# Performance work log

Hardware: AMD Instinct MI355X
Metric: run time of the kernel (lower is better)

Reference implementation:

```python
import jax, jax.numpy as jnp
import numpy as np

B, S, D = 64, 1024, 1024
NUM_TAGS = 33            # real IOBES tags
N = NUM_TAGS + 1         # + BOS tag
BOS = N - 1
NEG_INF = -10000.0


def setup_inputs() -> dict:
    key = jax.random.key(0)
    k1, k2, k3, k4 = jax.random.split(key, 4)
    emissions = jax.random.normal(k1, (B, S, D), dtype=jnp.float32)
    tags = jax.random.randint(k2, (B, S), 0, NUM_TAGS)          # valid real tags only
    mask = jnp.ones((B, S), dtype=jnp.float32)
    W = jax.random.normal(k3, (D, N), dtype=jnp.float32) / np.sqrt(D)
    b = jnp.zeros((N,), dtype=jnp.float32)
    transitions = jax.random.uniform(k4, (N, N), minval=-0.1, maxval=0.1, dtype=jnp.float32)
    # nothing may transition INTO the BOS tag
    transitions = transitions.at[:, BOS].set(NEG_INF)
    return {"emissions": emissions, "tags": tags, "mask": mask,
            "W": W, "b": b, "transitions": transitions}


def _crf_nll(em, tags, mask, transitions):
    """em: (B,S,N) projected emissions. Returns scalar NLL (sum over batch)."""
    # ---- gold path score ----
    first = tags[:, 0]                                          # (B,)
    score = transitions[BOS, first] + jnp.take_along_axis(em[:, 0], first[:, None], axis=1)[:, 0]
    e_t = jnp.take_along_axis(em[:, 1:], tags[:, 1:, None], axis=2)[..., 0]   # (B,S-1)
    t_t = transitions[tags[:, :-1], tags[:, 1:]]                 # (B,S-1)
    score = score + jnp.sum((e_t + t_t) * mask[:, 1:], axis=1)   # (B,)

    # ---- log partition via forward algorithm (scan over time) ----
    alphas0 = transitions[BOS][None, :] + em[:, 0]               # (B,N)

    def step(alphas, xs):
        em_t, m_t = xs                                           # (B,N), (B,)
        # scores[b, prev, nxt] = alphas[b,prev] + T[prev,nxt] + em_t[b,nxt]
        scores = alphas[:, :, None] + transitions[None] + em_t[:, None, :]
        new = jax.scipy.special.logsumexp(scores, axis=1)        # (B,N)
        m = m_t[:, None]
        return m * new + (1.0 - m) * alphas, None

    xs = (jnp.swapaxes(em[:, 1:], 0, 1), jnp.swapaxes(mask[:, 1:], 0, 1))  # time-major
    alphas, _ = jax.lax.scan(step, alphas0, xs)
    partition = jax.scipy.special.logsumexp(alphas, axis=1)      # (B,)
    return -jnp.sum(score - partition)


def reference(emissions, tags, mask, W, b, transitions):
    proj = emissions @ W + b                                     # (B,S,N), dropout p=0 is identity
    loss = _crf_nll(proj, tags, mask, transitions)
    logits = proj[:, :, :-1]                                     # drop BOS column, as in torch forward
    return loss, logits
```

## Files before the change

kernel.cpp:

```cpp
#include <hip/hip_runtime.h>
#include <math.h>

#define SS 1024
#define DD 1024
#define NB 64
#define NT 34
#define NP 48
#define NC 32
#define BOSR 33

typedef __attribute__((ext_vector_type(8))) short bf16x8;
typedef __attribute__((ext_vector_type(4))) float f32x4;

#define WS_BOS   0
#define WS_PMAT  (WS_BOS + NB*SS)
#define WS_CC    (WS_PMAT + NB*NC*NP*NP)
#define WS_Z     (WS_CC + NB*NC)
#define WS_SC    (WS_Z + NB)
#define WS_CNT   (WS_SC + NB)
#define WS_BF16  (WS_CNT + 1)
#define BW_WT    0
#define BW_ETA   (48*1024)

__device__ __forceinline__ float warp_sum64(float x) {
  #pragma unroll
  for (int off = 32; off > 0; off >>= 1) x += __shfl_down(x, off, 64);
  return x;
}
__device__ __forceinline__ float rfl(float x) {
  return __int_as_float(__builtin_amdgcn_readfirstlane(__float_as_int(x)));
}
__device__ __forceinline__ unsigned short f2bf(float f) {
  unsigned int u = __float_as_uint(f);
  unsigned int r = u + 0x7fffu + ((u >> 16) & 1u);
  return (unsigned short)(r >> 16);
}
__device__ __forceinline__ float bf2f(unsigned short h) {
  return __uint_as_float(((unsigned int)h) << 16);
}
__device__ __forceinline__ unsigned int pk_bf16(float a, float b) {
  unsigned int d;
  asm("v_cvt_pk_bf16_f32 %0, %1, %2" : "=v"(d) : "v"(a), "v"(b));
  return d;
}
__device__ __forceinline__ void lds_barrier() {
  asm volatile("s_waitcnt lgkmcnt(0)" ::: "memory");
  __builtin_amdgcn_s_barrier();
  __builtin_amdgcn_sched_barrier(0);
}

__global__ __launch_bounds__(256) void prep(const float* __restrict__ W,
                                            const float* __restrict__ T,
                                            unsigned short* __restrict__ bw,
                                            int* __restrict__ cnt) {
  int idx = blockIdx.x * 256 + threadIdx.x;
  if (idx == 0) *cnt = 0;
  if (idx < 48 * 1024) {
    int n = idx >> 10, k = idx & 1023;
    float v = (n < NT) ? W[k * NT + n] : 0.0f;
    bw[BW_WT + idx] = f2bf(v);
  } else if (idx < 48 * 1024 + 48 * 64) {
    int j = idx - 48 * 1024;
    int m = j >> 6, k = j & 63;
    float v = (m < NT && k < NT) ? __expf(T[k * NT + m]) : 0.0f;
    bw[BW_ETA + j] = f2bf(v);
  }
}

__global__ __launch_bounds__(256) void gemm_chains(
    const float* __restrict__ em, const unsigned short* __restrict__ bw,
    const float* __restrict__ bias, const float* __restrict__ mask,
    float* __restrict__ logits, float* __restrict__ bos,
    float* __restrict__ Pmat, float* __restrict__ CC) {
  union SMem {
    unsigned short At[2][128][40];
    struct {
      unsigned short S[4][48][72];
      float eeL[4][32][52];
    } ch;
  };
  __shared__ __align__(16) SMem sm;
  const int tid = threadIdx.x;
  const int lane = tid & 63, wv = tid >> 6;
  const int q = lane >> 4, l15 = lane & 15;
  const size_t row0 = (size_t)blockIdx.x * 128;
  const int b = (int)(row0 >> 10);
  const int cg = (((int)(row0 & 1023)) >> 5) + wv;
  const unsigned short* Wt = bw + BW_WT;
  const f32x4* g4 = (const f32x4*)(em + row0 * DD);

  f32x4 acc[2][3];
  f32x4 z4 = {0.f, 0.f, 0.f, 0.f};
  #pragma unroll
  for (int mt = 0; mt < 2; ++mt)
    #pragma unroll
    for (int nt = 0; nt < 3; ++nt) acc[mt][nt] = z4;

  int sr[4], sq[4];
  #pragma unroll
  for (int i = 0; i < 4; ++i) { int s = tid + i * 256; sr[i] = s >> 3; sq[i] = s & 7; }

  f32x4 pf[4];
  #pragma unroll
  for (int i = 0; i < 4; ++i)
    pf[i] = __builtin_nontemporal_load(g4 + sr[i] * 256 + sq[i]);
  bf16x8 Bf[3], Bn[3];
  #pragma unroll
  for (int nt = 0; nt < 3; ++nt)
    Bf[nt] = *(const bf16x8*)(Wt + (nt * 16 + l15) * 1024 + q * 8);

  for (int c = 0; c < 32; ++c) {
    #pragma unroll
    for (int i = 0; i < 4; ++i) {
      uint2 pk;
      pk.x = pk_bf16(pf[i][0], pf[i][1]);
      pk.y = pk_bf16(pf[i][2], pf[i][3]);
      *(uint2*)&sm.At[c & 1][sr[i]][sq[i] * 4] = pk;
    }
    int cn = (c + 1 < 32) ? c + 1 : c;
    #pragma unroll
    for (int i = 0; i < 4; ++i)
      pf[i] = __builtin_nontemporal_load(g4 + sr[i] * 256 + cn * 8 + sq[i]);
    #pragma unroll
    for (int nt = 0; nt < 3; ++nt)
      Bn[nt] = *(const bf16x8*)(Wt + (nt * 16 + l15) * 1024 + cn * 32 + q * 8);
    lds_barrier();
    bf16x8 Af[2];
    #pragma unroll
    for (int mt = 0; mt < 2; ++mt)
      Af[mt] = *(const bf16x8*)&sm.At[c & 1][wv * 32 + mt * 16 + l15][q * 8];
    #pragma unroll
    for (int mt = 0; mt < 2; ++mt)
      #pragma unroll
      for (int nt = 0; nt < 3; ++nt)
        acc[mt][nt] = __builtin_amdgcn_mfma_f32_16x16x32_bf16(
            Af[mt], Bf[nt], acc[mt][nt], 0, 0, 0);
    #pragma unroll
    for (int nt = 0; nt < 3; ++nt) Bf[nt] = Bn[nt];
  }

  __syncthreads();

  #pragma unroll
  for (int nt = 0; nt < 3; ++nt) {
    int col = nt * 16 + l15;
    float bj = (col < NT) ? bias[col] : 0.0f;
    #pragma unroll
    for (int mt = 0; mt < 2; ++mt) {
      #pragma unroll
      for (int r = 0; r < 4; ++r) {
        float v = acc[mt][nt][r] + bj;
        size_t rg = row0 + wv * 32 + mt * 16 + q * 4 + r;
        if (col < 33) logits[rg * 33 + col] = v;
        else if (col == 33) bos[rg] = v;
        sm.ch.eeL[wv][mt * 16 + q * 4 + r][col] = (col < NT) ? __expf(v) : 0.0f;
      }
    }
  }

  float mval = 0.0f;
  if (lane < 32) mval = mask[row0 + wv * 32 + lane];
  unsigned long long mb = __ballot(mval > 0.5f);
  if (cg == 0) mb &= ~1ull;

  {
    unsigned long long* p = (unsigned long long*)&sm.ch.S[wv][0][0];
    for (int i = lane; i < 864; i += 64) p[i] = 0ull;
  }
  if (lane < NT) sm.ch.S[wv][lane][lane] = 0x3F80;

  bf16x8 Ef[3][2];
  const unsigned short* eta = bw + BW_ETA;
  #pragma unroll
  for (int mt = 0; mt < 3; ++mt)
    #pragma unroll
    for (int kt = 0; kt < 2; ++kt)
      Ef[mt][kt] = *(const bf16x8*)(eta + (mt * 16 + l15) * 64 + kt * 32 + q * 8);

  float Clog = 0.0f;
  for (int tt = 0; tt < 32; ++tt) {
    if ((mb >> tt) & 1ull) {
      bf16x8 Bq[2][3];
      #pragma unroll
      for (int kt = 0; kt < 2; ++kt)
        #pragma unroll
        for (int nt = 0; nt < 3; ++nt)
          Bq[kt][nt] = *(const bf16x8*)&sm.ch.S[wv][nt * 16 + l15][kt * 32 + q * 8];
      f32x4 pacc[3][3];
      #pragma unroll
      for (int mt = 0; mt < 3; ++mt)
        #pragma unroll
        for (int nt = 0; nt < 3; ++nt) {
          pacc[mt][nt] = __builtin_amdgcn_mfma_f32_16x16x32_bf16(
              Ef[mt][0], Bq[0][nt], z4, 0, 0, 0);
          pacc[mt][nt] = __builtin_amdgcn_mfma_f32_16x16x32_bf16(
              Ef[mt][1], Bq[1][nt], pacc[mt][nt], 0, 0, 0);
        }
      float r = rfl(pacc[0][0][0]);
      float rin = __builtin_amdgcn_rcpf(r);
      Clog += __logf(r);
      #pragma unroll
      for (int mt = 0; mt < 3; ++mt) {
        f32x4 e4 = *(const f32x4*)&sm.ch.eeL[wv][tt][mt * 16 + q * 4];
        e4 = e4 * rin;
        #pragma unroll
        for (int nt = 0; nt < 3; ++nt) {
          f32x4 v = pacc[mt][nt] * e4;
          uint2 pk;
          pk.x = pk_bf16(v[0], v[1]);
          pk.y = pk_bf16(v[2], v[3]);
          *(uint2*)&sm.ch.S[wv][nt * 16 + l15][mt * 16 + q * 4] = pk;
        }
      }
    }
  }

  float* Pb = Pmat + (size_t)(b * NC + cg) * (NP * NP);
  #pragma unroll
  for (int i = 0; i < 9; ++i) {
    int flat = i * 64 + lane;
    int n = flat / 12, qq = flat - n * 12;
    unsigned long long pk = *(unsigned long long*)&sm.ch.S[wv][n][qq * 4];
    float4 o;
    o.x = bf2f((unsigned short)(pk));
    o.y = bf2f((unsigned short)(pk >> 16));
    o.z = bf2f((unsigned short)(pk >> 32));
    o.w = bf2f((unsigned short)(pk >> 48));
    *(float4*)&Pb[n * 48 + qq * 4] = o;
  }
  if (lane == 0) CC[b * NC + cg] = Clog;
}

__global__ __launch_bounds__(128) void reduceZ(
    const float* __restrict__ logits, const float* __restrict__ bos,
    const float* __restrict__ T, const float* __restrict__ Pmat,
    const float* __restrict__ CC, const int* __restrict__ tags,
    const float* __restrict__ mask, float* __restrict__ Zarr,
    float* __restrict__ scorearr, int* __restrict__ cnt,
    float* __restrict__ out) {
  const int b = blockIdx.x;
  const int tid = threadIdx.x;
  const int lane = tid & 63;
  __shared__ __align__(16) float shv[64];
  __shared__ int lastflag;

  if (tid >= 64) {
    float local = 0.0f;
    for (int t = lane; t < SS; t += 64) {
      if (t == 0) {
        int tg = tags[b * SS];
        local += T[BOSR * NT + tg] + logits[(size_t)(b * SS) * 33 + tg];
      } else {
        int tg = tags[b * SS + t];
        int tp = tags[b * SS + t - 1];
        float m = mask[b * SS + t];
        local += m * (logits[(size_t)(b * SS + t) * 33 + tg] + T[tp * NT + tg]);
      }
    }
    float w = warp_sum64(local);
    if (lane == 0) scorearr[b] = w;
  } else {
    float a0;
    if (lane < 33)       a0 = logits[(size_t)b * SS * 33 + lane] + T[BOSR * NT + lane];
    else if (lane == 33) a0 = bos[(size_t)b * SS] + T[BOSR * NT + 33];
    else                 a0 = -INFINITY;
    float K = rfl(a0);
    float v = (lane < 48) ? __expf(a0 - K) : 0.0f;
    float C = K;
    float CCl = (lane < 32) ? CC[b * NC + lane] : 0.0f;
    const float* Pbase = Pmat + (size_t)b * NC * (NP * NP) + lane * 48;

    f32x4 Pp[12];
    if (lane < 48) {
      #pragma unroll
      for (int i = 0; i < 12; ++i) Pp[i] = *(const f32x4*)(Pbase + i * 4);
    }
    for (int c = 0; c < NC; ++c) {
      shv[lane] = v;
      f32x4 cur[12];
      #pragma unroll
      for (int i = 0; i < 12; ++i) cur[i] = Pp[i];
      if (c + 1 < NC && lane < 48) {
        #pragma unroll
        for (int i = 0; i < 12; ++i)
          Pp[i] = *(const f32x4*)(Pbase + (size_t)(c + 1) * (NP * NP) + i * 4);
      }
      float u = 0.0f;
      if (lane < 48) {
        float uu0 = 0.f, uu1 = 0.f, uu2 = 0.f, uu3 = 0.f;
        #pragma unroll
        for (int qq = 0; qq < 12; qq += 4) {
          f32x4 v0 = *(const f32x4*)&shv[qq * 4];
          f32x4 v1 = *(const f32x4*)&shv[qq * 4 + 4];
          f32x4 v2 = *(const f32x4*)&shv[qq * 4 + 8];
          f32x4 v3 = *(const f32x4*)&shv[qq * 4 + 12];
          uu0 = fmaf(cur[qq][0], v0[0], uu0);   uu0 = fmaf(cur[qq][1], v0[1], uu0);
          uu0 = fmaf(cur[qq][2], v0[2], uu0);   uu0 = fmaf(cur[qq][3], v0[3], uu0);
          uu1 = fmaf(cur[qq+1][0], v1[0], uu1); uu1 = fmaf(cur[qq+1][1], v1[1], uu1);
          uu1 = fmaf(cur[qq+1][2], v1[2], uu1); uu1 = fmaf(cur[qq+1][3], v1[3], uu1);
          uu2 = fmaf(cur[qq+2][0], v2[0], uu2); uu2 = fmaf(cur[qq+2][1], v2[1], uu2);
          uu2 = fmaf(cur[qq+2][2], v2[2], uu2); uu2 = fmaf(cur[qq+2][3], v2[3], uu2);
          uu3 = fmaf(cur[qq+3][0], v3[0], uu3); uu3 = fmaf(cur[qq+3][1], v3[1], uu3);
          uu3 = fmaf(cur[qq+3][2], v3[2], uu3); uu3 = fmaf(cur[qq+3][3], v3[3], uu3);
        }
        u = (uu0 + uu1) + (uu2 + uu3);
      }
      float r = rfl(u);
      v = u * __builtin_amdgcn_rcpf(r);
      C += __logf(r) + __shfl(CCl, c, 64);
    }
    float s = warp_sum64(v);
    if (lane == 0) Zarr[b] = C + __logf(s);
  }

  __syncthreads();
  if (tid == 0) {
    __threadfence();
    lastflag = (atomicAdd(cnt, 1) == NB - 1);
  }
  __syncthreads();
  if (lastflag && tid < 64) {
    __threadfence();
    float x = Zarr[tid] - scorearr[tid];
    float s2 = warp_sum64(x);
    if (tid == 0) out[0] = s2;
  }
}

extern "C" void kernel_launch(void* const* d_in, const int* in_sizes, int n_in,
                              void* d_out, int out_size, void* d_ws, size_t ws_size,
                              hipStream_t stream) {
  const float* em   = (const float*)d_in[0];
  const int*   tags = (const int*)d_in[1];
  const float* mask = (const float*)d_in[2];
  const float* W    = (const float*)d_in[3];
  const float* bias = (const float*)d_in[4];
  const float* T    = (const float*)d_in[5];

  float* out = (float*)d_out;
  float* ws  = (float*)d_ws;
  float* bos   = ws + WS_BOS;
  float* Pmat  = ws + WS_PMAT;
  float* CC    = ws + WS_CC;
  float* Zarr  = ws + WS_Z;
  float* score = ws + WS_SC;
  int*   cnt   = (int*)(ws + WS_CNT);
  unsigned short* bw = (unsigned short*)(ws + WS_BF16);
  float* logits = out + 1;

  hipLaunchKernelGGL(prep, dim3(204), dim3(256), 0, stream, W, T, bw, cnt);
  hipLaunchKernelGGL(gemm_chains, dim3(NB * SS / 128), dim3(256), 0, stream,
                     em, bw, bias, mask, logits, bos, Pmat, CC);
  hipLaunchKernelGGL(reduceZ, dim3(NB), dim3(128), 0, stream,
                     logits, bos, T, Pmat, CC, tags, mask, Zarr, score, cnt, out);
}
```

Measured before the change: 415.7 us.

## Store chain transfer matrices as bf16 and double-buffer their loads in reduceZ

The per-chunk 48x48 transfer matrices are now written to workspace as raw bf16 instead of being widened to fp32, which halves the stores in gemm_chains and the loads in reduceZ. reduceZ unpacks the bf16 values in registers and prefetches two chunks ahead with ping-pong register buffers, so global load latency overlaps the serial chain combine. The values were already bf16-rounded, so numerics are unchanged, but register pressure and unpack ALU work rise in the latency-bound reduce loop.

```diff
diff --git a/kernel.cpp b/kernel.cpp
--- a/kernel.cpp
+++ b/kernel.cpp
@@ -11,10 +11,11 @@
 
 typedef __attribute__((ext_vector_type(8))) short bf16x8;
 typedef __attribute__((ext_vector_type(4))) float f32x4;
+typedef __attribute__((ext_vector_type(4))) unsigned int u32x4;
 
 #define WS_BOS   0
 #define WS_PMAT  (WS_BOS + NB*SS)
-#define WS_CC    (WS_PMAT + NB*NC*NP*NP)
+#define WS_CC    (WS_PMAT + NB*NC*1152)
 #define WS_Z     (WS_CC + NB*NC)
 #define WS_SC    (WS_Z + NB)
 #define WS_CNT   (WS_SC + NB)
@@ -35,8 +36,11 @@
   unsigned int r = u + 0x7fffu + ((u >> 16) & 1u);
   return (unsigned short)(r >> 16);
 }
-__device__ __forceinline__ float bf2f(unsigned short h) {
-  return __uint_as_float(((unsigned int)h) << 16);
+__device__ __forceinline__ float bflo(unsigned int d) {
+  return __uint_as_float(d << 16);
+}
+__device__ __forceinline__ float bfhi(unsigned int d) {
+  return __uint_as_float(d & 0xffff0000u);
 }
 __device__ __forceinline__ unsigned int pk_bf16(float a, float b) {
   unsigned int d;
@@ -71,7 +75,7 @@
     const float* __restrict__ em, const unsigned short* __restrict__ bw,
     const float* __restrict__ bias, const float* __restrict__ mask,
     float* __restrict__ logits, float* __restrict__ bos,
-    float* __restrict__ Pmat, float* __restrict__ CC) {
+    unsigned short* __restrict__ Pmat, float* __restrict__ CC) {
   union SMem {
     unsigned short At[2][128][40];
     struct {
@@ -215,25 +219,22 @@
     }
   }
 
-  float* Pb = Pmat + (size_t)(b * NC + cg) * (NP * NP);
-  #pragma unroll
-  for (int i = 0; i < 9; ++i) {
+  unsigned short* Pb = Pmat + (size_t)(b * NC + cg) * 2304;
+  #pragma unroll
+  for (int i = 0; i < 5; ++i) {
     int flat = i * 64 + lane;
-    int n = flat / 12, qq = flat - n * 12;
-    unsigned long long pk = *(unsigned long long*)&sm.ch.S[wv][n][qq * 4];
-    float4 o;
-    o.x = bf2f((unsigned short)(pk));
-    o.y = bf2f((unsigned short)(pk >> 16));
-    o.z = bf2f((unsigned short)(pk >> 32));
-    o.w = bf2f((unsigned short)(pk >> 48));
-    *(float4*)&Pb[n * 48 + qq * 4] = o;
+    if (flat < 288) {
+      int n = flat / 6, qq = flat - n * 6;
+      u32x4 d = *(const u32x4*)&sm.ch.S[wv][n][qq * 8];
+      *(u32x4*)(Pb + n * 48 + qq * 8) = d;
+    }
   }
   if (lane == 0) CC[b * NC + cg] = Clog;
 }
 
 __global__ __launch_bounds__(128) void reduceZ(
     const float* __restrict__ logits, const float* __restrict__ bos,
-    const float* __restrict__ T, const float* __restrict__ Pmat,
+    const float* __restrict__ T, const unsigned short* __restrict__ Pmat,
     const float* __restrict__ CC, const int* __restrict__ tags,
     const float* __restrict__ mask, float* __restrict__ Zarr,
     float* __restrict__ scorearr, int* __restrict__ cnt,
@@ -268,47 +269,61 @@
     float v = (lane < 48) ? __expf(a0 - K) : 0.0f;
     float C = K;
     float CCl = (lane < 32) ? CC[b * NC + lane] : 0.0f;
-    const float* Pbase = Pmat + (size_t)b * NC * (NP * NP) + lane * 48;
-
-    f32x4 Pp[12];
+    const unsigned short* Pr = Pmat + (size_t)b * NC * 2304 + lane * 48;
+
+    u32x4 PA[6], PB[6];
     if (lane < 48) {
       #pragma unroll
-      for (int i = 0; i < 12; ++i) Pp[i] = *(const f32x4*)(Pbase + i * 4);
-    }
-    for (int c = 0; c < NC; ++c) {
-      shv[lane] = v;
-      f32x4 cur[12];
-      #pragma unroll
-      for (int i = 0; i < 12; ++i) cur[i] = Pp[i];
-      if (c + 1 < NC && lane < 48) {
-        #pragma unroll
-        for (int i = 0; i < 12; ++i)
-          Pp[i] = *(const f32x4*)(Pbase + (size_t)(c + 1) * (NP * NP) + i * 4);
-      }
-      float u = 0.0f;
-      if (lane < 48) {
-        float uu0 = 0.f, uu1 = 0.f, uu2 = 0.f, uu3 = 0.f;
-        #pragma unroll
-        for (int qq = 0; qq < 12; qq += 4) {
-          f32x4 v0 = *(const f32x4*)&shv[qq * 4];
-          f32x4 v1 = *(const f32x4*)&shv[qq * 4 + 4];
-          f32x4 v2 = *(const f32x4*)&shv[qq * 4 + 8];
-          f32x4 v3 = *(const f32x4*)&shv[qq * 4 + 12];
-          uu0 = fmaf(cur[qq][0], v0[0], uu0);   uu0 = fmaf(cur[qq][1], v0[1], uu0);
-          uu0 = fmaf(cur[qq][2], v0[2], uu0);   uu0 = fmaf(cur[qq][3], v0[3], uu0);
-          uu1 = fmaf(cur[qq+1][0], v1[0], uu1); uu1 = fmaf(cur[qq+1][1], v1[1], uu1);
-          uu1 = fmaf(cur[qq+1][2], v1[2], uu1); uu1 = fmaf(cur[qq+1][3], v1[3], uu1);
-          uu2 = fmaf(cur[qq+2][0], v2[0], uu2); uu2 = fmaf(cur[qq+2][1], v2[1], uu2);
-          uu2 = fmaf(cur[qq+2][2], v2[2], uu2); uu2 = fmaf(cur[qq+2][3], v2[3], uu2);
-          uu3 = fmaf(cur[qq+3][0], v3[0], uu3); uu3 = fmaf(cur[qq+3][1], v3[1], uu3);
-          uu3 = fmaf(cur[qq+3][2], v3[2], uu3); uu3 = fmaf(cur[qq+3][3], v3[3], uu3);
-        }
-        u = (uu0 + uu1) + (uu2 + uu3);
-      }
-      float r = rfl(u);
-      v = u * __builtin_amdgcn_rcpf(r);
-      C += __logf(r) + __shfl(CCl, c, 64);
-    }
+      for (int i = 0; i < 6; ++i) PA[i] = *(const u32x4*)(Pr + i * 8);
+      #pragma unroll
+      for (int i = 0; i < 6; ++i) PB[i] = *(const u32x4*)(Pr + 2304 + i * 8);
+    }
+
+    #define COMBINE(BUF, c)                                                    \
+    {                                                                          \
+      shv[lane] = v;                                    \
+      float u = 0.0f;                                                          \
+      if (lane < 48) {                                                         \
+        float uu0 = 0.f, uu1 = 0.f, uu2 = 0.f, uu3 = 0.f;                      \
+        _Pragma("unroll")                                                      \
+        for (int g = 0; g < 3; ++g) {                                          \
+          u32x4 Pa = BUF[2 * g], Pc = BUF[2 * g + 1];                          \
+          f32x4 v0 = *(const f32x4*)&shv[g * 16];                              \
+          f32x4 v1 = *(const f32x4*)&shv[g * 16 + 4];                          \
+          f32x4 v2 = *(const f32x4*)&shv[g * 16 + 8];                          \
+          f32x4 v3 = *(const f32x4*)&shv[g * 16 + 12];                         \
+          uu0 = fmaf(bflo(Pa[0]), v0[0], uu0); uu0 = fmaf(bfhi(Pa[0]), v0[1], uu0); \
+          uu0 = fmaf(bflo(Pa[1]), v0[2], uu0); uu0 = fmaf(bfhi(Pa[1]), v0[3], uu0); \
+          uu1 = fmaf(bflo(Pa[2]), v1[0], uu1); uu1 = fmaf(bfhi(Pa[2]), v1[1], uu1); \
+          uu1 = fmaf(bflo(Pa[3]), v1[2], uu1); uu1 = fmaf(bfhi(Pa[3]), v1[3], uu1); \
+          uu2 = fmaf(bflo(Pc[0]), v2[0], uu2); uu2 = fmaf(bfhi(Pc[0]), v2[1], uu2); \
+          uu2 = fmaf(bflo(Pc[1]), v2[2], uu2); uu2 = fmaf(bfhi(Pc[1]), v2[3], uu2); \
+          uu3 = fmaf(bflo(Pc[2]), v3[0], uu3); uu3 = fmaf(bfhi(Pc[2]), v3[1], uu3); \
+          uu3 = fmaf(bflo(Pc[3]), v3[2], uu3); uu3 = fmaf(bfhi(Pc[3]), v3[3], uu3); \
+        }                                                                      \
+        u = (uu0 + uu1) + (uu2 + uu3);                                         \
+      }                                                                        \
+      float r = rfl(u);                                                        \
+      v = u * __builtin_amdgcn_rcpf(r);                                        \
+      C += __logf(r) + __shfl(CCl, (c), 64);                                   \
+    }
+
+    for (int cc = 0; cc < NC / 2; ++cc) {
+      int c0 = 2 * cc;
+      COMBINE(PA, c0);
+      if (c0 + 2 < NC && lane < 48) {
+        #pragma unroll
+        for (int i = 0; i < 6; ++i)
+          PA[i] = *(const u32x4*)(Pr + (size_t)(c0 + 2) * 2304 + i * 8);
+      }
+      COMBINE(PB, c0 + 1);
+      if (c0 + 3 < NC && lane < 48) {
+        #pragma unroll
+        for (int i = 0; i < 6; ++i)
+          PB[i] = *(const u32x4*)(Pr + (size_t)(c0 + 3) * 2304 + i * 8);
+      }
+    }
+    #undef COMBINE
     float s = warp_sum64(v);
     if (lane == 0) Zarr[b] = C + __logf(s);
   }
@@ -340,7 +355,7 @@
   float* out = (float*)d_out;
   float* ws  = (float*)d_ws;
   float* bos   = ws + WS_BOS;
-  float* Pmat  = ws + WS_PMAT;
+  unsigned short* Pmat16 = (unsigned short*)(ws + WS_PMAT);
   float* CC    = ws + WS_CC;
   float* Zarr  = ws + WS_Z;
   float* score = ws + WS_SC;
@@ -350,7 +365,7 @@
 
   hipLaunchKernelGGL(prep, dim3(204), dim3(256), 0, stream, W, T, bw, cnt);
   hipLaunchKernelGGL(gemm_chains, dim3(NB * SS / 128), dim3(256), 0, stream,
-                     em, bw, bias, mask, logits, bos, Pmat, CC);
+                     em, bw, bias, mask, logits, bos, Pmat16, CC);
   hipLaunchKernelGGL(reduceZ, dim3(NB), dim3(128), 0, stream,
-                     logits, bos, T, Pmat, CC, tags, mask, Zarr, score, cnt, out);
-}
+                     logits, bos, T, Pmat16, CC, tags, mask, Zarr, score, cnt, out);
+}
```

Measured after the change: 409.7 us. No clear change (-1.4%).
